# Performance work log

Hardware: AMD Instinct MI355X
Metric: run time of the kernel (lower is better)

Reference implementation:

```python
import jax, jax.numpy as jnp
import numpy as np

NUM_GROUPS = 32
EPS = 1e-5


def setup_inputs() -> dict:
    key = jax.random.key(0)
    ks = jax.random.split(key, 6)
    B, C, H, W = 8, 128, 64, 64
    d = C // 8
    x = jax.random.normal(ks[0], (B, C, H, W), dtype=jnp.float32)
    # conv 1x1 weights stored as [out_ch, in_ch]; scaled like torch kaiming-uniform-ish
    s = 1.0 / np.sqrt(C)
    return {
        "x": x,
        "gn_w": jnp.ones((C,), jnp.float32),
        "gn_b": jnp.zeros((C,), jnp.float32),
        "q_w": jax.random.normal(ks[1], (d, C), jnp.float32) * s,
        "q_b": jnp.zeros((d,), jnp.float32),
        "k_w": jax.random.normal(ks[2], (d, C), jnp.float32) * s,
        "k_b": jnp.zeros((d,), jnp.float32),
        "v_w": jax.random.normal(ks[3], (C, C), jnp.float32) * s,
        "v_b": jnp.zeros((C,), jnp.float32),
        "p_w": jax.random.normal(ks[4], (C, C), jnp.float32) * s,
        "p_b": jnp.zeros((C,), jnp.float32),
    }


def _group_norm(x, w, b):
    B, C, H, W = x.shape
    g = NUM_GROUPS
    xr = x.reshape(B, g, C // g, H, W)
    mu = xr.mean(axis=(2, 3, 4), keepdims=True)
    var = xr.var(axis=(2, 3, 4), keepdims=True)
    xn = ((xr - mu) * jax.lax.rsqrt(var + EPS)).reshape(B, C, H, W)
    return xn * w[None, :, None, None] + b[None, :, None, None]


def reference(x, gn_w, gn_b, q_w, q_b, k_w, k_b, v_w, v_b, p_w, p_b):
    B, C, H, W = x.shape
    N = H * W
    h_ = _group_norm(x, gn_w, gn_b)            # [B,C,H,W]
    hf = h_.reshape(B, C, N)                   # flatten spatial
    # 1x1 convs == channel matmuls
    q = jnp.einsum('dc,bcn->bnd', q_w, hf) + q_b[None, None, :]   # [B,N,d]
    k = jnp.einsum('dc,bcn->bnd', k_w, hf) + k_b[None, None, :]   # [B,N,d]
    v = jnp.einsum('ec,bcn->ben', v_w, hf) + v_b[None, :, None]   # [B,C,N]
    d = q.shape[-1]
    scale = jnp.asarray(int(d) ** (-0.5), x.dtype)
    attn = jnp.einsum('bid,bjd->bij', q, k) * scale               # [B,N,N]
    attn = jax.nn.softmax(attn, axis=-1)
    a = jnp.einsum('bcj,bij->bci', v, attn)                       # [B,C,N]
    proj = jnp.einsum('ec,bcn->ben', p_w, a) + p_b[None, :, None]
    return x + proj.reshape(B, C, H, W)
```

## Files before the change

### kernel.cpp

```cpp
#include <hip/hip_runtime.h>
#include <math.h>


typedef short v8s __attribute__((ext_vector_type(8)));
typedef float v16f __attribute__((ext_vector_type(16)));

__device__ __forceinline__ unsigned short f2bf_rne(float f) {
  unsigned u = __float_as_uint(f);
  u += 0x7fffu + ((u >> 16) & 1u);
  return (unsigned short)(u >> 16);
}

__device__ __forceinline__ v8s mk8(unsigned a, unsigned b, unsigned c, unsigned d) {
  union { unsigned u[4]; v8s s; } x;
  x.u[0] = a; x.u[1] = b; x.u[2] = c; x.u[3] = d;
  return x.s;
}

__device__ __forceinline__ unsigned pack_trunc(float hi, float lo) {
  return __builtin_amdgcn_perm(__float_as_uint(hi), __float_as_uint(lo), 0x07060302u);
}

#define VT(b, n, c) (((((size_t)(b) * 256 + ((n) >> 4)) << 7) + (c)) * 16 + ((n) & 15))

#define WSB_MURS   0u
#define WSB_WCATB  4096u
#define WSB_BCAT   49152u
#define WSB_PWB    65536u
#define WSB_QBF    131072u
#define WSB_KBF    1310720u
#define WSB_VBF    2621440u
#define WSB_ABF    11534336u

__global__ void prep_kernel(const float* __restrict__ qw, const float* __restrict__ qb,
                            const float* __restrict__ kw, const float* __restrict__ kb,
                            const float* __restrict__ vw, const float* __restrict__ vb,
                            const float* __restrict__ pw,
                            unsigned short* __restrict__ wcatb, float* __restrict__ bcat,
                            unsigned short* __restrict__ pwb) {
  const float qs = 0.36067376022224085f;
  int idx = blockIdx.x * 256 + threadIdx.x;
  if (idx < 160 * 128) {
    int o = idx >> 7, c = idx & 127;
    float val;
    if (o < 16)       val = qw[o * 128 + c] * qs;
    else if (o < 32)  val = kw[(o - 16) * 128 + c];
    else              val = vw[(o - 32) * 128 + c];
    wcatb[idx] = f2bf_rne(val);
  } else if (idx < 160 * 128 + 160) {
    int o = idx - 160 * 128;
    bcat[o] = (o < 16) ? qb[o] * qs : (o < 32) ? kb[o - 16] : vb[o - 32];
  } else if (idx < 160 * 128 + 160 + 128 * 128) {
    int j = idx - (160 * 128 + 160);
    pwb[j] = f2bf_rne(pw[j]);
  }
}

__global__ __launch_bounds__(512)
void gn_stats_kernel(const float* __restrict__ x, float* __restrict__ mu_rs) {
  const int id = blockIdx.x;
  const int bg = (id & 7) * 32 + (id >> 3);
  const float4* xp = (const float4*)(x + (size_t)bg * 16384);
  float s = 0.f, ss = 0.f;
#pragma unroll
  for (int u = 0; u < 8; ++u) {
    int i = threadIdx.x + u * 512;
    float4 v = xp[i];
    s  += v.x + v.y + v.z + v.w;
    ss += v.x * v.x + v.y * v.y + v.z * v.z + v.w * v.w;
  }
  for (int off = 32; off > 0; off >>= 1) {
    s  += __shfl_down(s, off, 64);
    ss += __shfl_down(ss, off, 64);
  }
  __shared__ float red[16];
  int lane = threadIdx.x & 63, wid = threadIdx.x >> 6;
  if (lane == 0) { red[wid * 2] = s; red[wid * 2 + 1] = ss; }
  __syncthreads();
  if (threadIdx.x == 0) {
    float S = 0.f, SS = 0.f;
    for (int w = 0; w < 8; ++w) { S += red[w * 2]; SS += red[w * 2 + 1]; }
    float mu  = S * (1.0f / 16384.0f);
    float var = SS * (1.0f / 16384.0f) - mu * mu;
    float rs  = rsqrtf(var + 1e-5f);
    mu_rs[bg * 2]     = mu;
    mu_rs[bg * 2 + 1] = rs;
  }
}

__global__ __launch_bounds__(512)
void qkv_kernel(const float* __restrict__ x, const float* __restrict__ gnw,
                const float* __restrict__ gnb, const float* __restrict__ mu_rs,
                const unsigned short* __restrict__ wcatb, const float* __restrict__ bcat,
                unsigned short* __restrict__ qbf, unsigned short* __restrict__ kbf,
                unsigned short* __restrict__ vbf) {
  __shared__ float scs[128], shs[128], bsh[160];
  const int id = blockIdx.x;
  const int b = id & 7, nb = (id >> 3) << 6;
  const int t = threadIdx.x;
  const int w = t >> 6, lane = t & 63, h = lane >> 5, l = lane & 31;
  const int nsub = w & 1, og = w >> 1;
  if (t < 128) {
    float mu = mu_rs[(b * 32 + (t >> 2)) * 2];
    float rs = mu_rs[(b * 32 + (t >> 2)) * 2 + 1];
    float gw = gnw[t], gb = gnb[t];
    scs[t] = rs * gw; shs[t] = gb - mu * rs * gw;
  }
  if (t < 160) bsh[t] = bcat[t];
  __syncthreads();

  const int n = nb + nsub * 32 + l;
  const float* xb = x + ((size_t)b * 128 << 12);
  const int otbase = (og == 0) ? 0 : og + 1;

  float xv[64];
#pragma unroll
  for (int ks = 0; ks < 8; ++ks)
#pragma unroll
    for (int p = 0; p < 8; ++p)
      xv[ks * 8 + p] = xb[((size_t)(ks * 16 + 8 * h + p) << 12) + n];

  v16f acc[2];
#pragma unroll
  for (int a2 = 0; a2 < 2; ++a2)
#pragma unroll
    for (int r = 0; r < 16; ++r) acc[a2][r] = 0.f;

#pragma unroll
  for (int ks = 0; ks < 8; ++ks) {
    const int c0 = ks * 16 + 8 * h;
    unsigned fd[4];
#pragma unroll
    for (int p = 0; p < 4; ++p) {
      int ca = c0 + 2 * p;
      float h0 = xv[ks * 8 + 2 * p]     * scs[ca]     + shs[ca];
      float h1 = xv[ks * 8 + 2 * p + 1] * scs[ca + 1] + shs[ca + 1];
      fd[p] = (unsigned)f2bf_rne(h0) | ((unsigned)f2bf_rne(h1) << 16);
    }
    v8s bf = mk8(fd[0], fd[1], fd[2], fd[3]);
    {
      v8s af = *(const v8s*)(wcatb + (otbase * 32 + l) * 128 + ks * 16 + 8 * h);
      acc[0] = __builtin_amdgcn_mfma_f32_32x32x16_bf16(af, bf, acc[0], 0, 0, 0);
    }
    if (og == 0) {
      v8s af = *(const v8s*)(wcatb + (32 + l) * 128 + ks * 16 + 8 * h);
      acc[1] = __builtin_amdgcn_mfma_f32_32x32x16_bf16(af, bf, acc[1], 0, 0, 0);
    }
  }

  if (og == 0) {
    const size_t nqk = ((size_t)b * 4096 + n) << 4;
#pragma unroll
    for (int r = 0; r < 16; ++r) {
      int o = 4 * h + (r & 3) + 8 * (r >> 2);
      unsigned short bv = f2bf_rne(acc[0][r] + bsh[o]);
      if (o < 16) qbf[nqk + o] = bv; else kbf[nqk + o - 16] = bv;
    }
#pragma unroll
    for (int r = 0; r < 16; ++r) {
      int o = 32 + 4 * h + (r & 3) + 8 * (r >> 2);
      vbf[VT(b, n, o - 32)] = f2bf_rne(acc[1][r] + bsh[o]);
    }
  } else {
#pragma unroll
    for (int r = 0; r < 16; ++r) {
      int o = otbase * 32 + 4 * h + (r & 3) + 8 * (r >> 2);
      vbf[VT(b, n, o - 32)] = f2bf_rne(acc[0][r] + bsh[o]);
    }
  }
}

#define VS 40
#define KOFF (512 * VS)

__global__ __launch_bounds__(512)
void attn_kernel(const unsigned short* __restrict__ qbf,
                 const unsigned short* __restrict__ kbf,
                 const unsigned short* __restrict__ vbf,
                 unsigned short* __restrict__ abf) {
  __shared__ alignas(16) unsigned short kvs[KOFF + 64 * VS];
  __shared__ alignas(16) unsigned short pbuf[128 * 72];
  __shared__ float l_lds[128];

  const int id = blockIdx.x;
  const int b = id & 7, i0 = (id >> 3) << 7;
  const int t = threadIdx.x;
  const int w = t >> 6, lane = t & 63, h = lane >> 5, l = lane & 31;
  const int jsub = w & 1, iquad = w >> 1;
  const int ipair = w & 1, ct = w >> 1;

  const unsigned short* kg = kbf + ((size_t)b << 16);
  const unsigned short* vg = vbf + ((size_t)b << 19);

  const v8s qf = *(const v8s*)(qbf + (((size_t)(b * 4096 + i0 + iquad * 32 + l)) << 4) + 8 * h);

  v16f zc;
#pragma unroll
  for (int r = 0; r < 16; ++r) zc[r] = 0.f;
  v16f acc0, acc1;
#pragma unroll
  for (int r = 0; r < 16; ++r) { acc0[r] = 0.f; acc1[r] = 0.f; }
  float ls = 0.f;

  const int vrow = w * 64 + (lane >> 1);
  const int sh16 = (lane & 1) * 8;
  const int krow = (w & 1) * 32 + (lane >> 1);

  if (t < 128) l_lds[t] = 0.f;

  for (int tile = 0; tile < 64; ++tile) {
    v8s s0 = *(const v8s*)(vg + (size_t)tile * 8192 + vrow * 16 + sh16);
    v8s s1 = *(const v8s*)(vg + (size_t)tile * 8192 + (vrow + 32) * 16 + sh16);
    v8s sk = {};
    if (w < 2) sk = *(const v8s*)(kg + (size_t)tile * 1024 + krow * 16 + sh16);

    __syncthreads();

    *(v8s*)(kvs + vrow * VS + sh16) = s0;
    *(v8s*)(kvs + (vrow + 32) * VS + sh16) = s1;
    if (w < 2) *(v8s*)(kvs + KOFF + krow * VS + sh16) = sk;

    __syncthreads();

    v8s kf = *(const v8s*)(kvs + KOFF + (jsub * 32 + l) * VS + 8 * h);
    v16f st = __builtin_amdgcn_mfma_f32_32x32x16_bf16(kf, qf, zc, 0, 0, 0);
    float pe[16];
#pragma unroll
    for (int r = 0; r < 16; ++r) { pe[r] = __builtin_amdgcn_exp2f(st[r]); ls += pe[r]; }
    {
      unsigned* prow = (unsigned*)(pbuf + (iquad * 32 + l) * 72);
#pragma unroll
      for (int q = 0; q < 4; ++q) {
        const int jq = jsub * 32 + 4 * h + 8 * q;
        prow[(jq >> 1)]     = pack_trunc(pe[4 * q + 1], pe[4 * q]);
        prow[(jq >> 1) + 1] = pack_trunc(pe[4 * q + 3], pe[4 * q + 2]);
      }
    }

    __syncthreads();

#pragma unroll
    for (int ks = 0; ks < 4; ++ks) {
      v8s vf  = *(const v8s*)(kvs + (ks * 128 + ct * 32 + l) * VS + 8 * h);
      v8s pfa = *(const v8s*)(pbuf + ((ipair * 2)     * 32 + l) * 72 + ks * 16 + 8 * h);
      v8s pfb = *(const v8s*)(pbuf + ((ipair * 2 + 1) * 32 + l) * 72 + ks * 16 + 8 * h);
      acc0 = __builtin_amdgcn_mfma_f32_32x32x16_bf16(vf, pfa, acc0, 0, 0, 0);
      acc1 = __builtin_amdgcn_mfma_f32_32x32x16_bf16(vf, pfb, acc1, 0, 0, 0);
    }
  }

  atomicAdd(&l_lds[iquad * 32 + l], ls);
  __syncthreads();
  const float li0 = 1.f / l_lds[ipair * 64 + l];
  const float li1 = 1.f / l_lds[ipair * 64 + 32 + l];
#pragma unroll
  for (int r = 0; r < 16; ++r) {
    int c = ct * 32 + 4 * h + (r & 3) + 8 * (r >> 2);
    size_t base = ((size_t)(b * 128 + c) << 12) + i0 + ipair * 64 + l;
    abf[base]      = f2bf_rne(acc0[r] * li0);
    abf[base + 32] = f2bf_rne(acc1[r] * li1);
  }
}

__global__ __launch_bounds__(512)
void proj_kernel(const unsigned short* __restrict__ abf, const unsigned short* __restrict__ pwb,
                 const float* __restrict__ pb, const float* __restrict__ x,
                 float* __restrict__ out) {
  __shared__ float pbs[128];
  const int id = blockIdx.x;
  const int b = id & 7, nb = (id >> 3) << 6;
  const int t = threadIdx.x;
  const int w = t >> 6, lane = t & 63, h = lane >> 5, l = lane & 31;
  const int nsub = w & 1, ot = w >> 1;
  if (t < 128) pbs[t] = pb[t];
  __syncthreads();

  const int n = nb + nsub * 32 + l;
  const unsigned short* ab = abf + (((size_t)b * 128) << 12);

  unsigned short av[64];
#pragma unroll
  for (int ks = 0; ks < 8; ++ks)
#pragma unroll
    for (int p = 0; p < 8; ++p)
      av[ks * 8 + p] = ab[((size_t)(ks * 16 + 8 * h + p) << 12) + n];

  v16f acc;
#pragma unroll
  for (int r = 0; r < 16; ++r) acc[r] = 0.f;

#pragma unroll
  for (int ks = 0; ks < 8; ++ks) {
    unsigned fd[4];
#pragma unroll
    for (int p = 0; p < 4; ++p)
      fd[p] = (unsigned)av[ks * 8 + 2 * p] | ((unsigned)av[ks * 8 + 2 * p + 1] << 16);
    v8s bf = mk8(fd[0], fd[1], fd[2], fd[3]);
    v8s af = *(const v8s*)(pwb + (ot * 32 + l) * 128 + ks * 16 + 8 * h);
    acc = __builtin_amdgcn_mfma_f32_32x32x16_bf16(af, bf, acc, 0, 0, 0);
  }

#pragma unroll
  for (int r = 0; r < 16; ++r) {
    int e = ot * 32 + 4 * h + (r & 3) + 8 * (r >> 2);
    size_t idx = ((size_t)(b * 128 + e) << 12) + n;
    out[idx] = acc[r] + pbs[e] + x[idx];
  }
}

extern "C" void kernel_launch(void* const* d_in, const int* in_sizes, int n_in,
                              void* d_out, int out_size, void* d_ws, size_t ws_size,
                              hipStream_t stream) {
  const float* x   = (const float*)d_in[0];
  const float* gnw = (const float*)d_in[1];
  const float* gnb = (const float*)d_in[2];
  const float* qw  = (const float*)d_in[3];
  const float* qb  = (const float*)d_in[4];
  const float* kw  = (const float*)d_in[5];
  const float* kb  = (const float*)d_in[6];
  const float* vw  = (const float*)d_in[7];
  const float* vb  = (const float*)d_in[8];
  const float* pw  = (const float*)d_in[9];
  const float* pb  = (const float*)d_in[10];
  float* out = (float*)d_out;
  char* ws = (char*)d_ws;

  float* mu_rs = (float*)(ws + WSB_MURS);
  unsigned short* wcatb = (unsigned short*)(ws + WSB_WCATB);
  float* bcat = (float*)(ws + WSB_BCAT);
  unsigned short* pwb = (unsigned short*)(ws + WSB_PWB);
  unsigned short* qbf = (unsigned short*)(ws + WSB_QBF);
  unsigned short* kbf = (unsigned short*)(ws + WSB_KBF);
  unsigned short* vbf = (unsigned short*)(ws + WSB_VBF);
  unsigned short* abf = (unsigned short*)(ws + WSB_ABF);

  hipLaunchKernelGGL(prep_kernel, dim3(145), dim3(256), 0, stream,
                     qw, qb, kw, kb, vw, vb, pw, wcatb, bcat, pwb);
  hipLaunchKernelGGL(gn_stats_kernel, dim3(256), dim3(512), 0, stream, x, mu_rs);
  hipLaunchKernelGGL(qkv_kernel, dim3(512), dim3(512), 0, stream,
                     x, gnw, gnb, mu_rs, wcatb, bcat, qbf, kbf, vbf);
  hipLaunchKernelGGL(attn_kernel, dim3(256), dim3(512), 0, stream,
                     qbf, kbf, vbf, abf);
  hipLaunchKernelGGL(proj_kernel, dim3(512), dim3(512), 0, stream,
                     abf, pwb, pb, x, out);
}
```

Measured before the change: 177.7 us.

## Keep P in registers via lane shuffles and split PV over key halves

The attention kernel now loads K fragments straight from global memory instead of staging them in LDS. The bf16 probabilities are exchanged between half-waves with shuffles to form the PV operand directly, so the P buffer in LDS goes away. One barrier per tile is removed, and each wave now accumulates all 128 channels for its own query quad over half the keys. The two key halves are summed through a shared-memory reduction at the end. This trades LDS traffic and syncs for more accumulator registers (64 floats per lane) and a 64KB shared buffer, which may lower occupancy.

```diff
diff --git a/kernel.cpp b/kernel.cpp
--- a/kernel.cpp
+++ b/kernel.cpp
@@ -171,23 +171,22 @@
 }
 
 #define VS 40
-#define KOFF (512 * VS)
 
 __global__ __launch_bounds__(512)
 void attn_kernel(const unsigned short* __restrict__ qbf,
                  const unsigned short* __restrict__ kbf,
                  const unsigned short* __restrict__ vbf,
                  unsigned short* __restrict__ abf) {
-  __shared__ alignas(16) unsigned short kvs[KOFF + 64 * VS];
-  __shared__ alignas(16) unsigned short pbuf[128 * 72];
+  __shared__ alignas(16) unsigned char smemb[65536];
   __shared__ float l_lds[128];
+  unsigned short* const vlds = (unsigned short*)smemb;
+  float* const comb = (float*)smemb;
 
   const int id = blockIdx.x;
   const int b = id & 7, i0 = (id >> 3) << 7;
   const int t = threadIdx.x;
   const int w = t >> 6, lane = t & 63, h = lane >> 5, l = lane & 31;
   const int jsub = w & 1, iquad = w >> 1;
-  const int ipair = w & 1, ct = w >> 1;
 
   const unsigned short* kg = kbf + ((size_t)b << 16);
   const unsigned short* vg = vbf + ((size_t)b << 19);
@@ -197,68 +196,92 @@
   v16f zc;
 #pragma unroll
   for (int r = 0; r < 16; ++r) zc[r] = 0.f;
-  v16f acc0, acc1;
-#pragma unroll
-  for (int r = 0; r < 16; ++r) { acc0[r] = 0.f; acc1[r] = 0.f; }
+  v16f acc[4];
+#pragma unroll
+  for (int ct = 0; ct < 4; ++ct)
+#pragma unroll
+    for (int r = 0; r < 16; ++r) acc[ct][r] = 0.f;
   float ls = 0.f;
 
   const int vrow = w * 64 + (lane >> 1);
   const int sh16 = (lane & 1) * 8;
-  const int krow = (w & 1) * 32 + (lane >> 1);
 
   if (t < 128) l_lds[t] = 0.f;
 
   for (int tile = 0; tile < 64; ++tile) {
     v8s s0 = *(const v8s*)(vg + (size_t)tile * 8192 + vrow * 16 + sh16);
     v8s s1 = *(const v8s*)(vg + (size_t)tile * 8192 + (vrow + 32) * 16 + sh16);
-    v8s sk = {};
-    if (w < 2) sk = *(const v8s*)(kg + (size_t)tile * 1024 + krow * 16 + sh16);
+    v8s kf = *(const v8s*)(kg + (((size_t)(tile * 64 + jsub * 32 + l)) << 4) + 8 * h);
 
     __syncthreads();
 
-    *(v8s*)(kvs + vrow * VS + sh16) = s0;
-    *(v8s*)(kvs + (vrow + 32) * VS + sh16) = s1;
-    if (w < 2) *(v8s*)(kvs + KOFF + krow * VS + sh16) = sk;
-
-    __syncthreads();
-
-    v8s kf = *(const v8s*)(kvs + KOFF + (jsub * 32 + l) * VS + 8 * h);
+    *(v8s*)(vlds + vrow * VS + sh16) = s0;
+    *(v8s*)(vlds + (vrow + 32) * VS + sh16) = s1;
+
     v16f st = __builtin_amdgcn_mfma_f32_32x32x16_bf16(kf, qf, zc, 0, 0, 0);
     float pe[16];
 #pragma unroll
     for (int r = 0; r < 16; ++r) { pe[r] = __builtin_amdgcn_exp2f(st[r]); ls += pe[r]; }
-    {
-      unsigned* prow = (unsigned*)(pbuf + (iquad * 32 + l) * 72);
+    unsigned G[8];
+#pragma unroll
+    for (int g = 0; g < 4; ++g) {
+      G[2 * g]     = pack_trunc(pe[4 * g + 1], pe[4 * g]);
+      G[2 * g + 1] = pack_trunc(pe[4 * g + 3], pe[4 * g + 2]);
+    }
+    unsigned S0 = h ? G[0] : G[2], S1 = h ? G[1] : G[3];
+    unsigned S2 = h ? G[4] : G[6], S3 = h ? G[5] : G[7];
+    unsigned R0 = (unsigned)__shfl_xor((int)S0, 32, 64);
+    unsigned R1 = (unsigned)__shfl_xor((int)S1, 32, 64);
+    unsigned R2 = (unsigned)__shfl_xor((int)S2, 32, 64);
+    unsigned R3 = (unsigned)__shfl_xor((int)S3, 32, 64);
+    v8s pf0 = h ? mk8(R0, R1, G[2], G[3]) : mk8(G[0], G[1], R0, R1);
+    v8s pf1 = h ? mk8(R2, R3, G[6], G[7]) : mk8(G[4], G[5], R2, R3);
+
+    __syncthreads();
+
+#pragma unroll
+    for (int ct = 0; ct < 4; ++ct) {
+      v8s vf0 = *(const v8s*)(vlds + ((jsub * 2) * 128 + ct * 32 + l) * VS + 8 * h);
+      v8s vf1 = *(const v8s*)(vlds + ((jsub * 2 + 1) * 128 + ct * 32 + l) * VS + 8 * h);
+      acc[ct] = __builtin_amdgcn_mfma_f32_32x32x16_bf16(vf0, pf0, acc[ct], 0, 0, 0);
+      acc[ct] = __builtin_amdgcn_mfma_f32_32x32x16_bf16(vf1, pf1, acc[ct], 0, 0, 0);
+    }
+  }
+
+  atomicAdd(&l_lds[iquad * 32 + l], ls);
+  __syncthreads();
+
+  float* const myreg = comb + iquad * 4096;
+  if (jsub == 1) {
+#pragma unroll
+    for (int ct = 0; ct < 4; ++ct)
 #pragma unroll
       for (int q = 0; q < 4; ++q) {
-        const int jq = jsub * 32 + 4 * h + 8 * q;
-        prow[(jq >> 1)]     = pack_trunc(pe[4 * q + 1], pe[4 * q]);
-        prow[(jq >> 1) + 1] = pack_trunc(pe[4 * q + 3], pe[4 * q + 2]);
+        float4 v4 = {acc[ct][4 * q], acc[ct][4 * q + 1],
+                     acc[ct][4 * q + 2], acc[ct][4 * q + 3]};
+        *(float4*)&myreg[ct * 1024 + lane * 16 + 4 * q] = v4;
       }
-    }
-
-    __syncthreads();
-
-#pragma unroll
-    for (int ks = 0; ks < 4; ++ks) {
-      v8s vf  = *(const v8s*)(kvs + (ks * 128 + ct * 32 + l) * VS + 8 * h);
-      v8s pfa = *(const v8s*)(pbuf + ((ipair * 2)     * 32 + l) * 72 + ks * 16 + 8 * h);
-      v8s pfb = *(const v8s*)(pbuf + ((ipair * 2 + 1) * 32 + l) * 72 + ks * 16 + 8 * h);
-      acc0 = __builtin_amdgcn_mfma_f32_32x32x16_bf16(vf, pfa, acc0, 0, 0, 0);
-      acc1 = __builtin_amdgcn_mfma_f32_32x32x16_bf16(vf, pfb, acc1, 0, 0, 0);
-    }
-  }
-
-  atomicAdd(&l_lds[iquad * 32 + l], ls);
-  __syncthreads();
-  const float li0 = 1.f / l_lds[ipair * 64 + l];
-  const float li1 = 1.f / l_lds[ipair * 64 + 32 + l];
-#pragma unroll
-  for (int r = 0; r < 16; ++r) {
-    int c = ct * 32 + 4 * h + (r & 3) + 8 * (r >> 2);
-    size_t base = ((size_t)(b * 128 + c) << 12) + i0 + ipair * 64 + l;
-    abf[base]      = f2bf_rne(acc0[r] * li0);
-    abf[base + 32] = f2bf_rne(acc1[r] * li1);
+  }
+  __syncthreads();
+  if (jsub == 0) {
+    const float li = 1.f / l_lds[iquad * 32 + l];
+#pragma unroll
+    for (int ct = 0; ct < 4; ++ct) {
+#pragma unroll
+      for (int q = 0; q < 4; ++q) {
+        float4 v4 = *(float4*)&myreg[ct * 1024 + lane * 16 + 4 * q];
+        acc[ct][4 * q]     += v4.x;
+        acc[ct][4 * q + 1] += v4.y;
+        acc[ct][4 * q + 2] += v4.z;
+        acc[ct][4 * q + 3] += v4.w;
+      }
+#pragma unroll
+      for (int r = 0; r < 16; ++r) {
+        int c = ct * 32 + 4 * h + (r & 3) + 8 * (r >> 2);
+        abf[((size_t)(b * 128 + c) << 12) + i0 + iquad * 32 + l] =
+            f2bf_rne(acc[ct][r] * li);
+      }
+    }
   }
 }
 
```

New measurement: 171.0 us. -3.8%, faster.
